# Performance work log

Hardware: AMD Instinct MI355X
Metric: run time of the kernel (lower is better)

## Reference

```python
import jax, jax.numpy as jnp
import numpy as np

EPS = 1e-8  # torch cosine_similarity eps


def setup_inputs() -> dict:
    key = jax.random.key(0)
    kq, km = jax.random.split(key)
    B, N, D = 256, 100000, 1024
    query = jax.random.normal(kq, (B, D), dtype=jnp.float32)
    memory = jax.random.normal(km, (N, D), dtype=jnp.float32)
    return {"query": query, "memory": memory, "k": 16}


def reference(query, memory, k):
    # Batched, fused version of HierarchicalMemory.retrieve():
    # cosine similarity of each query against every stored module, then top-k.
    # sim(q, m) = q.m / max(||q||*||m||, eps), matching F.cosine_similarity.
    qn = jnp.linalg.norm(query, axis=-1)          # [B]
    mn = jnp.linalg.norm(memory, axis=-1)         # [N]
    dots = jnp.einsum("bd,nd->bn", query, memory)  # [B, N]
    sims = dots / jnp.maximum(qn[:, None] * mn[None, :], EPS)
    top_vals, top_idx = jax.lax.top_k(sims, k)    # [B, k] each
    return top_vals, top_idx
```

## Files before the change

kernel.cpp:

```cpp
#include <hip/hip_runtime.h>
#include <math.h>

#define DDIM 1024
#define BQ 256
#define EPSV 1e-8f
#define CH 4
#define TPC 32
#define NCAND (CH * TPC)

typedef short bf16x8 __attribute__((ext_vector_type(8)));
typedef float f32x4 __attribute__((ext_vector_type(4)));

__device__ __forceinline__ unsigned short f2bf(float x) {
  union { float f; unsigned int u; } v;
  v.f = x;
  unsigned int lsb = (v.u >> 16) & 1u;
  v.u += 0x7fffu + lsb;
  return (unsigned short)(v.u >> 16);
}
__device__ __forceinline__ float bf2f(unsigned short b) {
  union { unsigned int u; float f; } v;
  v.u = ((unsigned int)b) << 16;
  return v.f;
}

#define ASYNC_CP16(gp, lp)                                                     \
  __builtin_amdgcn_global_load_lds(                                            \
      (const __attribute__((address_space(1))) unsigned int*)(const void*)(gp),\
      (__attribute__((address_space(3))) unsigned int*)(lp), 16, 0, 0)

__global__ __launch_bounds__(256) void prep_q(const float* __restrict__ Q,
                                              unsigned short* __restrict__ Qb,
                                              float* __restrict__ qn) {
  int wave = threadIdx.x >> 6, lane = threadIdx.x & 63;
  int q = blockIdx.x * 4 + wave;
  const float4* src = (const float4*)(Q + (size_t)q * DDIM);
  unsigned short* dst = Qb + (size_t)q * DDIM;
  float s = 0.f;
#pragma unroll
  for (int t = 0; t < 4; ++t) {
    float4 v = src[t * 64 + lane];
    s += v.x * v.x + v.y * v.y + v.z * v.z + v.w * v.w;
    ushort4 o;
    o.x = f2bf(v.x); o.y = f2bf(v.y); o.z = f2bf(v.z); o.w = f2bf(v.w);
    *(ushort4*)(dst + t * 256 + lane * 4) = o;
  }
#pragma unroll
  for (int o = 32; o > 0; o >>= 1) s += __shfl_down(s, o, 64);
  if (lane == 0) qn[q] = sqrtf(s);
}

__global__ __launch_bounds__(256) void gemm_topk(
    const float* __restrict__ M, const unsigned short* __restrict__ Qb,
    unsigned short* __restrict__ sims, float* __restrict__ rmn,
    int N, int Npitch) {
  __shared__ unsigned short Qs[256 * 32];
  __shared__ unsigned short Ms[64 * 32];
  const int tid = threadIdx.x;
  const int wave = tid >> 6, lane = tid & 63;
  const int quad = lane >> 4, l15 = lane & 15;
  const int n0 = blockIdx.x * 64;

  const int mrow = tid >> 2;
  const int mchunk = tid & 3;
  const bool mvalid = (n0 + mrow) < N;
  const float* mptr = M + (size_t)(mvalid ? (n0 + mrow) : 0) * DDIM + mchunk * 8;

  f32x4 acc[4][4];
#pragma unroll
  for (int i = 0; i < 4; ++i)
#pragma unroll
    for (int j = 0; j < 4; ++j) acc[i][j] = (f32x4){0.f, 0.f, 0.f, 0.f};
  float sumsq = 0.f;

  for (int k0 = 0; k0 < DDIM; k0 += 32) {
    float4 m0, m1;
    if (mvalid) {
      m0 = *(const float4*)(mptr + k0);
      m1 = *(const float4*)(mptr + k0 + 4);
    } else {
      m0 = make_float4(0.f, 0.f, 0.f, 0.f);
      m1 = m0;
    }
    __syncthreads();
#pragma unroll
    for (int r = 0; r < 4; ++r) {
      int row0 = r * 64 + wave * 16;
      const unsigned short* g =
          Qb + (size_t)(row0 + (lane >> 2)) * DDIM + k0 + (lane & 3) * 8;
      ASYNC_CP16(g, &Qs[row0 * 32]);
    }
    sumsq += m0.x * m0.x + m0.y * m0.y + m0.z * m0.z + m0.w * m0.w +
             m1.x * m1.x + m1.y * m1.y + m1.z * m1.z + m1.w * m1.w;
    uint4 packed;
    packed.x = (unsigned int)f2bf(m0.x) | ((unsigned int)f2bf(m0.y) << 16);
    packed.y = (unsigned int)f2bf(m0.z) | ((unsigned int)f2bf(m0.w) << 16);
    packed.z = (unsigned int)f2bf(m1.x) | ((unsigned int)f2bf(m1.y) << 16);
    packed.w = (unsigned int)f2bf(m1.z) | ((unsigned int)f2bf(m1.w) << 16);
    *(uint4*)&Ms[mrow * 32 + mchunk * 8] = packed;
    __syncthreads();
    bf16x8 afr[4], bfr[4];
#pragma unroll
    for (int i = 0; i < 4; ++i)
      afr[i] = *(const bf16x8*)&Qs[(wave * 64 + i * 16 + l15) * 32 + quad * 8];
#pragma unroll
    for (int j = 0; j < 4; ++j)
      bfr[j] = *(const bf16x8*)&Ms[(j * 16 + l15) * 32 + quad * 8];
#pragma unroll
    for (int i = 0; i < 4; ++i)
#pragma unroll
      for (int j = 0; j < 4; ++j)
        acc[i][j] = __builtin_amdgcn_mfma_f32_16x16x32_bf16(afr[i], bfr[j],
                                                            acc[i][j], 0, 0, 0);
  }

  float s = sumsq;
  s += __shfl_xor(s, 1, 64);
  s += __shfl_xor(s, 2, 64);
  if (mchunk == 0) rmn[n0 + mrow] = (s > 0.f) ? rsqrtf(s) : 0.f;

#pragma unroll
  for (int i = 0; i < 4; ++i)
#pragma unroll
    for (int j = 0; j < 4; ++j)
#pragma unroll
      for (int r = 0; r < 4; ++r) {
        int q = wave * 64 + i * 16 + quad * 4 + r;
        int n = n0 + j * 16 + l15;
        sims[(size_t)q * Npitch + n] = f2bf(acc[i][j][r]);
      }
}

__device__ __forceinline__ bool better(float v1, int i1, float v2, int i2) {
  return v1 > v2 || (v1 == v2 && i1 < i2);
}

template <int L>
__device__ __forceinline__ void insert_topL(float (&tv)[L], int (&ti)[L],
                                            float v, int idx) {
  if (v > tv[L - 1] || (v == tv[L - 1] && idx < ti[L - 1])) {
    tv[L - 1] = v; ti[L - 1] = idx;
#pragma unroll
    for (int j = L - 1; j > 0; --j) {
      if (better(tv[j], ti[j], tv[j - 1], ti[j - 1])) {
        float fv = tv[j]; tv[j] = tv[j - 1]; tv[j - 1] = fv;
        int ii = ti[j]; ti[j] = ti[j - 1]; ti[j - 1] = ii;
      }
    }
  }
}

template <int L, typename F>
__device__ __forceinline__ void block_extract(float (&tv)[L], int (&ti)[L],
                                              int rounds, F&& emit) {
  __shared__ float s_v[4];
  __shared__ int s_i[4];
  __shared__ int s_t[4];
  __shared__ float s_wv;
  __shared__ int s_wi;
  __shared__ int s_wt;
  for (int r = 0; r < rounds; ++r) {
    float v = tv[0];
    int idx = ti[0];
    int src = threadIdx.x;
#pragma unroll
    for (int o = 32; o > 0; o >>= 1) {
      float ov = __shfl_down(v, o, 64);
      int oi = __shfl_down(idx, o, 64);
      int os = __shfl_down(src, o, 64);
      if (better(ov, oi, v, idx)) { v = ov; idx = oi; src = os; }
    }
    int lane = threadIdx.x & 63, w = threadIdx.x >> 6;
    if (lane == 0) { s_v[w] = v; s_i[w] = idx; s_t[w] = src; }
    __syncthreads();
    if (threadIdx.x == 0) {
      float bv = s_v[0]; int bi = s_i[0]; int bt = s_t[0];
      for (int w2 = 1; w2 < 4; ++w2)
        if (better(s_v[w2], s_i[w2], bv, bi)) { bv = s_v[w2]; bi = s_i[w2]; bt = s_t[w2]; }
      s_wv = bv; s_wi = bi; s_wt = bt;
    }
    __syncthreads();
    if (threadIdx.x == s_wt) {
#pragma unroll
      for (int j = 0; j < L - 1; ++j) { tv[j] = tv[j + 1]; ti[j] = ti[j + 1]; }
      tv[L - 1] = -INFINITY; ti[L - 1] = 0x7fffffff;
    }
    if (threadIdx.x == 0) emit(r, s_wv, s_wi);
    __syncthreads();
  }
}

__global__ __launch_bounds__(256) void select_chunks(
    const unsigned short* __restrict__ sims, const float* __restrict__ rmn,
    int* __restrict__ cand, int N, int Npitch, int Nc) {
  int q = blockIdx.y;
  int c = blockIdx.x;
  int start = c * Nc;
  int end = start + Nc;
  if (end > N) end = N;
  float tv[8]; int ti[8];
#pragma unroll
  for (int j = 0; j < 8; ++j) { tv[j] = -INFINITY; ti[j] = 0x7fffffff; }
  const unsigned short* row = sims + (size_t)q * Npitch;
  int base = start + threadIdx.x * 8;
  for (; base + 8 <= end; base += 2048) {
    uint4 wv = *(const uint4*)(row + base);
    float4 r0 = *(const float4*)&rmn[base];
    float4 r1 = *(const float4*)&rmn[base + 4];
    float f0 = bf2f((unsigned short)(wv.x & 0xffff)) * r0.x;
    float f1 = bf2f((unsigned short)(wv.x >> 16)) * r0.y;
    float f2 = bf2f((unsigned short)(wv.y & 0xffff)) * r0.z;
    float f3 = bf2f((unsigned short)(wv.y >> 16)) * r0.w;
    float f4 = bf2f((unsigned short)(wv.z & 0xffff)) * r1.x;
    float f5 = bf2f((unsigned short)(wv.z >> 16)) * r1.y;
    float f6 = bf2f((unsigned short)(wv.w & 0xffff)) * r1.z;
    float f7 = bf2f((unsigned short)(wv.w >> 16)) * r1.w;
    insert_topL<8>(tv, ti, f0, base + 0);
    insert_topL<8>(tv, ti, f1, base + 1);
    insert_topL<8>(tv, ti, f2, base + 2);
    insert_topL<8>(tv, ti, f3, base + 3);
    insert_topL<8>(tv, ti, f4, base + 4);
    insert_topL<8>(tv, ti, f5, base + 5);
    insert_topL<8>(tv, ti, f6, base + 6);
    insert_topL<8>(tv, ti, f7, base + 7);
  }
  if (base < end) {
    for (int n = base; n < end; ++n)
      insert_topL<8>(tv, ti, bf2f(row[n]) * rmn[n], n);
  }
  int* dst = cand + (size_t)q * NCAND + c * TPC;
  block_extract<8>(tv, ti, TPC, [&](int r, float v, int i) {
    dst[r] = (i == 0x7fffffff) ? 0 : i;
  });
}

__global__ __launch_bounds__(512) void rescore(
    const float* __restrict__ Q, const float* __restrict__ M,
    const float* __restrict__ qn, const int* __restrict__ cand,
    float* __restrict__ out, int N) {
  __shared__ float cosv[NCAND];
  __shared__ int cidx[NCAND];
  int q = blockIdx.x;
  int wave = threadIdx.x >> 6, lane = threadIdx.x & 63;
  const float4* qf4 = (const float4*)(Q + (size_t)q * DDIM);
  float4 qv[4];
#pragma unroll
  for (int t = 0; t < 4; ++t) qv[t] = qf4[t * 64 + lane];
  float qnv = qn[q];
#pragma unroll 1
  for (int i = 0; i < NCAND / 8; ++i) {
    int c = wave * (NCAND / 8) + i;
    int idx = cand[(size_t)q * NCAND + c];
    if (idx < 0 || idx >= N) idx = 0;
    const float4* mf4 = (const float4*)(M + (size_t)idx * DDIM);
    float dot = 0.f, sq = 0.f;
#pragma unroll
    for (int t = 0; t < 4; ++t) {
      float4 m = mf4[t * 64 + lane];
      dot += m.x * qv[t].x + m.y * qv[t].y + m.z * qv[t].z + m.w * qv[t].w;
      sq += m.x * m.x + m.y * m.y + m.z * m.z + m.w * m.w;
    }
#pragma unroll
    for (int o = 32; o > 0; o >>= 1) {
      dot += __shfl_down(dot, o, 64);
      sq += __shfl_down(sq, o, 64);
    }
    if (lane == 0) {
      cosv[c] = dot / fmaxf(qnv * sqrtf(sq), EPSV);
      cidx[c] = idx;
    }
  }
  __syncthreads();
  if (wave == 0) {
    float v0 = cosv[lane], v1 = cosv[lane + 64];
    int i0 = cidx[lane], i1 = cidx[lane + 64];
    for (int r = 0; r < 16; ++r) {
      bool fb = better(v0, i0, v1, i1);
      float bv = fb ? v0 : v1;
      int bi = fb ? i0 : i1;
      int bs = lane * 2 + (fb ? 0 : 1);
#pragma unroll
      for (int o = 32; o > 0; o >>= 1) {
        float ov = __shfl_down(bv, o, 64);
        int oi = __shfl_down(bi, o, 64);
        int os = __shfl_down(bs, o, 64);
        if (better(ov, oi, bv, bi)) { bv = ov; bi = oi; bs = os; }
      }
      bv = __shfl(bv, 0, 64);
      bi = __shfl(bi, 0, 64);
      bs = __shfl(bs, 0, 64);
      if (lane == (bs >> 1)) {
        if (bs & 1) v1 = -INFINITY; else v0 = -INFINITY;
      }
      if (lane == 0) {
        out[(size_t)q * 16 + r] = bv;
        out[(size_t)BQ * 16 + (size_t)q * 16 + r] = (float)bi;
      }
    }
  }
}

extern "C" void kernel_launch(void* const* d_in, const int* in_sizes, int n_in,
                              void* d_out, int out_size, void* d_ws, size_t ws_size,
                              hipStream_t stream) {
  const float* Q = (const float*)d_in[0];
  const float* M = (const float*)d_in[1];
  int N = in_sizes[1] / DDIM;
  float* out = (float*)d_out;

  int nb = (N + 63) / 64;
  int Npitch = nb * 64;

  char* w = (char*)d_ws;
  size_t off = 0;
  auto alloc = [&](size_t bytes) {
    char* p = w + off;
    off = (off + bytes + 255) & ~(size_t)255;
    return p;
  };
  unsigned short* Qb = (unsigned short*)alloc((size_t)BQ * DDIM * 2);
  float* qn = (float*)alloc((size_t)BQ * 4);
  float* rmn = (float*)alloc((size_t)Npitch * 4);
  int* cand = (int*)alloc((size_t)BQ * NCAND * 4);
  unsigned short* sims = (unsigned short*)alloc((size_t)BQ * Npitch * 2);
  (void)ws_size;

  int Nc = (((N + CH - 1) / CH) + 7) & ~7;

  prep_q<<<BQ / 4, 256, 0, stream>>>(Q, Qb, qn);
  gemm_topk<<<nb, 256, 0, stream>>>(M, Qb, sims, rmn, N, Npitch);
  select_chunks<<<dim3(CH, BQ), 256, 0, stream>>>(sims, rmn, cand, N, Npitch, Nc);
  rescore<<<BQ, 512, 0, stream>>>(Q, M, qn, cand, out, N);
}
```

Baseline: 739.2 us.

## Double-buffer Q and M tiles with register prefetch and single barrier per step

```diff
diff --git a/kernel.cpp b/kernel.cpp
--- a/kernel.cpp
+++ b/kernel.cpp
@@ -22,6 +22,11 @@
   union { unsigned int u; float f; } v;
   v.u = ((unsigned int)b) << 16;
   return v.f;
+}
+__device__ __forceinline__ unsigned int cvtpk_bf16(float lo, float hi) {
+  unsigned int r;
+  asm("v_cvt_pk_bf16_f32 %0, %1, %2" : "=v"(r) : "v"(lo), "v"(hi));
+  return r;
 }
 
 #define ASYNC_CP16(gp, lp)                                                     \
@@ -54,8 +59,8 @@
     const float* __restrict__ M, const unsigned short* __restrict__ Qb,
     unsigned short* __restrict__ sims, float* __restrict__ rmn,
     int N, int Npitch) {
-  __shared__ unsigned short Qs[256 * 32];
-  __shared__ unsigned short Ms[64 * 32];
+  __shared__ unsigned short Qs[2][256 * 32];
+  __shared__ unsigned short Ms[2][64 * 32];
   const int tid = threadIdx.x;
   const int wave = tid >> 6, lane = tid & 63;
   const int quad = lane >> 4, l15 = lane & 15;
@@ -73,45 +78,59 @@
     for (int j = 0; j < 4; ++j) acc[i][j] = (f32x4){0.f, 0.f, 0.f, 0.f};
   float sumsq = 0.f;
 
-  for (int k0 = 0; k0 < DDIM; k0 += 32) {
-    float4 m0, m1;
-    if (mvalid) {
-      m0 = *(const float4*)(mptr + k0);
-      m1 = *(const float4*)(mptr + k0 + 4);
-    } else {
-      m0 = make_float4(0.f, 0.f, 0.f, 0.f);
-      m1 = m0;
-    }
-    __syncthreads();
+  auto stageQ = [&](int k0, int buf) {
 #pragma unroll
     for (int r = 0; r < 4; ++r) {
       int row0 = r * 64 + wave * 16;
       const unsigned short* g =
           Qb + (size_t)(row0 + (lane >> 2)) * DDIM + k0 + (lane & 3) * 8;
-      ASYNC_CP16(g, &Qs[row0 * 32]);
-    }
-    sumsq += m0.x * m0.x + m0.y * m0.y + m0.z * m0.z + m0.w * m0.w +
-             m1.x * m1.x + m1.y * m1.y + m1.z * m1.z + m1.w * m1.w;
+      ASYNC_CP16(g, &Qs[buf][row0 * 32]);
+    }
+  };
+
+  stageQ(0, 0);
+  float4 mrA0 = *(const float4*)(mptr);
+  float4 mrA1 = *(const float4*)(mptr + 4);
+  float4 mrB0 = *(const float4*)(mptr + 32);
+  float4 mrB1 = *(const float4*)(mptr + 36);
+
+  auto body = [&](int t, int buf, float4& r0, float4& r1) {
+    sumsq += r0.x * r0.x + r0.y * r0.y + r0.z * r0.z + r0.w * r0.w +
+             r1.x * r1.x + r1.y * r1.y + r1.z * r1.z + r1.w * r1.w;
     uint4 packed;
-    packed.x = (unsigned int)f2bf(m0.x) | ((unsigned int)f2bf(m0.y) << 16);
-    packed.y = (unsigned int)f2bf(m0.z) | ((unsigned int)f2bf(m0.w) << 16);
-    packed.z = (unsigned int)f2bf(m1.x) | ((unsigned int)f2bf(m1.y) << 16);
-    packed.w = (unsigned int)f2bf(m1.z) | ((unsigned int)f2bf(m1.w) << 16);
-    *(uint4*)&Ms[mrow * 32 + mchunk * 8] = packed;
-    __syncthreads();
+    packed.x = cvtpk_bf16(r0.x, r0.y);
+    packed.y = cvtpk_bf16(r0.z, r0.w);
+    packed.z = cvtpk_bf16(r1.x, r1.y);
+    packed.w = cvtpk_bf16(r1.z, r1.w);
+    *(uint4*)&Ms[buf][mrow * 32 + mchunk * 8] = packed;
+    int k2 = t * 32 + 64;
+    const float* p = mptr + ((k2 < DDIM) ? k2 : 0);
+    r0 = *(const float4*)(p);
+    r1 = *(const float4*)(p + 4);
+    asm volatile("s_waitcnt vmcnt(2) lgkmcnt(0)" ::: "memory");
+    __builtin_amdgcn_s_barrier();
+    __builtin_amdgcn_sched_barrier(0);
+    if (t < 31) stageQ(t * 32 + 32, buf ^ 1);
     bf16x8 afr[4], bfr[4];
 #pragma unroll
     for (int i = 0; i < 4; ++i)
-      afr[i] = *(const bf16x8*)&Qs[(wave * 64 + i * 16 + l15) * 32 + quad * 8];
+      afr[i] =
+          *(const bf16x8*)&Qs[buf][(wave * 64 + i * 16 + l15) * 32 + quad * 8];
 #pragma unroll
     for (int j = 0; j < 4; ++j)
-      bfr[j] = *(const bf16x8*)&Ms[(j * 16 + l15) * 32 + quad * 8];
+      bfr[j] = *(const bf16x8*)&Ms[buf][(j * 16 + l15) * 32 + quad * 8];
 #pragma unroll
     for (int i = 0; i < 4; ++i)
 #pragma unroll
       for (int j = 0; j < 4; ++j)
         acc[i][j] = __builtin_amdgcn_mfma_f32_16x16x32_bf16(afr[i], bfr[j],
                                                             acc[i][j], 0, 0, 0);
+  };
+
+#pragma unroll 1
+  for (int t = 0; t < 32; t += 2) {
+    body(t, 0, mrA0, mrA1);
+    body(t + 1, 1, mrB0, mrB1);
   }
 
   float s = sumsq;
```

Measured after the change: 722.7 us. -2.2%, faster.
